# Optimization experiments

Measured on AMD Instinct MI355X. Metric: run time of the kernel, lower is better.

## Reference

```python
import jax, jax.numpy as jnp
import numpy as np
from jax import lax

V, E, Hd = 128, 256, 1024
B, S = 32, 1024

def setup_inputs() -> dict:
    key = jax.random.key(0)
    ks = jax.random.split(key, 10)
    s = 0.02
    return {
        "x": jax.random.randint(ks[0], (B, S), 0, V),
        "emb": jax.random.normal(ks[1], (V, E), jnp.float32) * s,
        "Wx_w": jax.random.normal(ks[2], (Hd, E), jnp.float32) * s,
        "Wx_b": jnp.zeros((Hd,), jnp.float32),
        "Wh_w": jax.random.normal(ks[3], (Hd, Hd), jnp.float32) * s,
        "Wh_b": jnp.zeros((Hd,), jnp.float32),
        "Wa_w": jax.random.normal(ks[4], (Hd, Hd), jnp.float32) * s,
        "Wa_b": jnp.zeros((Hd,), jnp.float32),
        "fc_w": jax.random.normal(ks[5], (V, 2 * Hd), jnp.float32) * s,
        "fc_b": jnp.zeros((V,), jnp.float32),
    }

def reference(x, emb, Wx_w, Wx_b, Wh_w, Wh_b, Wa_w, Wa_b, fc_w, fc_b):
    b, s = x.shape
    xe = emb[x]                                    # [B,S,E]
    Xp = jnp.einsum('bse,he->bsh', xe, Wx_w) + Wx_b  # precomputed input projection

    def step(h, xp_t):                             # h: [B,Hd], xp_t: [B,Hd]
        h2 = jnp.tanh(xp_t + h @ Wh_w.T + Wh_b)
        return h2, h2

    h0 = jnp.zeros((b, Wh_w.shape[0]), Xp.dtype)
    _, Hs = lax.scan(step, h0, Xp.transpose(1, 0, 2))  # [S,B,Hd]
    H = Hs.transpose(1, 0, 2)                      # [B,S,Hd]

    A = H @ Wa_w.T + Wa_b                          # W_a(H), computed once
    # scores[b,s,t] = A[b,s] . H[b,t]; key axis s, query axis t
    scores = jnp.einsum('bsh,bth->bst', A, H)
    allowed = jnp.triu(jnp.ones((s, s), bool))     # s <= t allowed (causal)
    scores = jnp.where(allowed[None], scores, -jnp.inf)
    weights = jax.nn.softmax(scores, axis=1)       # softmax over keys s
    context = jnp.einsum('bst,bsh->bth', weights, H)  # [B,S,Hd]

    combined = jnp.concatenate([H, context], axis=-1)  # [B,S,2Hd]
    return combined @ fc_w.T + fc_b                # [B,S,V]
```

## Files before the change

kernel.cpp:

```cpp
#include <hip/hip_runtime.h>
#include <hip/hip_bf16.h>
#include <hip/hip_cooperative_groups.h>

#define NV 128
#define NE 256
#define HD 1024
#define NB 32
#define NS 1024

typedef unsigned short u16;
typedef unsigned long long u64;
typedef unsigned short ushort8 __attribute__((ext_vector_type(8)));
typedef unsigned short u16x4 __attribute__((ext_vector_type(4)));
typedef short bf16x8 __attribute__((ext_vector_type(8)));
typedef float f32x4 __attribute__((ext_vector_type(4)));

#define MFMA16(a, b, c) __builtin_amdgcn_mfma_f32_16x16x32_bf16(a, b, c, 0, 0, 0)

__device__ __forceinline__ float bf2f(u16 u){
  unsigned int x = ((unsigned int)u) << 16;
  return __builtin_bit_cast(float, x);
}
__device__ __forceinline__ u16 f2bf(float f){
  unsigned int u = __builtin_bit_cast(unsigned int, f);
  unsigned int r = u + 0x7fffu + ((u >> 16) & 1u);
  return (u16)(r >> 16);
}

__global__ __launch_bounds__(256) void k_cvt(const float* __restrict__ waw,
    const float* __restrict__ fcw, u16* __restrict__ wa_bf, u16* __restrict__ fc_bf)
{
  const int i = blockIdx.x * 256 + threadIdx.x;
  if (i < 1048576) wa_bf[i] = f2bf(waw[i]);
  const int j = i - 1048576;
  if (j >= 0 && j < 262144) fc_bf[j] = f2bf(fcw[j]);
}

__global__ __launch_bounds__(256) void k_xw(const float* __restrict__ emb,
    const float* __restrict__ wxw, const float* __restrict__ wxb,
    float* __restrict__ XW)
{
  __shared__ float es[NE];
  const int v = blockIdx.x;
  for (int i = threadIdx.x; i < NE; i += 256) es[i] = emb[v*NE + i];
  __syncthreads();
  for (int h = threadIdx.x; h < HD; h += 256){
    const float* wr = wxw + (size_t)h * NE;
    float acc = 0.f;
#pragma unroll 4
    for (int e = 0; e < NE; e += 4){
      float4 w4 = *reinterpret_cast<const float4*>(wr + e);
      acc += w4.x*es[e] + w4.y*es[e+1] + w4.z*es[e+2] + w4.w*es[e+3];
    }
    XW[(size_t)v*HD + h] = acc + wxb[h];
  }
}

__global__ __launch_bounds__(256, 1) void k_scan2(const int* __restrict__ x,
    const float* __restrict__ whw, const float* __restrict__ whb,
    const float* __restrict__ XW, u64* __restrict__ hstate,
    u16* __restrict__ Harc)
{
  __shared__ __align__(16) float hs[4096];
  __shared__ int xs[4096];
  const int tid = threadIdx.x;
  const int g = blockIdx.x & 7;
  const int m = blockIdx.x >> 3;
  const int kc = tid & 31;
  const int rg = tid >> 5;
  const int row0 = m*32 + rg*4;

  for (int i = tid; i < 4096; i += 256) xs[i] = x[g*4096 + i];

  float4 wv[4][8];
#pragma unroll
  for (int r = 0; r < 4; ++r)
#pragma unroll
    for (int j = 0; j < 8; ++j)
      wv[r][j] = *reinterpret_cast<const float4*>(
          whw + (size_t)(row0 + r)*HD + kc*32 + ((4*(j + kc)) & 31));

  const int rr = row0 + (kc & 3);
  const int bb = kc >> 2;
  const float bias = whb[rr];
  __syncthreads();

  for (int t = 0; t < NS; ++t){
    const u64* hin  = hstate + (size_t)(t & 1)*(NB*HD) + g*4*HD;
    u64*       hout = hstate + (size_t)((t & 1)^1)*(NB*HD) + g*4*HD;
    const unsigned tg = (unsigned)t;
    u64 v[16];
#pragma unroll
    for (int q = 0; q < 16; ++q)
      v[q] = __hip_atomic_load(hin + q*256 + tid, __ATOMIC_RELAXED,
                               __HIP_MEMORY_SCOPE_AGENT);
    for (;;){
      bool ok = true;
#pragma unroll
      for (int q = 0; q < 16; ++q)
        if ((unsigned)(v[q] >> 32) != tg){
          ok = false;
          v[q] = __hip_atomic_load(hin + q*256 + tid, __ATOMIC_RELAXED,
                                   __HIP_MEMORY_SCOPE_AGENT);
        }
      if (ok) break;
      __builtin_amdgcn_s_sleep(1);
    }
#pragma unroll
    for (int q = 0; q < 16; ++q)
      hs[q*256 + tid] = __builtin_bit_cast(float, (unsigned)v[q]);
    float xwv = 0.f;
    if (kc < 16){
      const int xv = xs[bb*1024 + t];
      xwv = XW[(size_t)xv*HD + rr];
    }
    __syncthreads();

    float acc[4][4] = {};
#pragma unroll
    for (int j = 0; j < 8; ++j){
      const int off = kc*32 + ((4*(j + kc)) & 31);
      float4 h4[4];
#pragma unroll
      for (int b = 0; b < 4; ++b)
        h4[b] = *reinterpret_cast<const float4*>(&hs[b*1024 + off]);
#pragma unroll
      for (int r = 0; r < 4; ++r)
#pragma unroll
        for (int b = 0; b < 4; ++b)
          acc[r][b] += wv[r][j].x*h4[b].x + wv[r][j].y*h4[b].y
                     + wv[r][j].z*h4[b].z + wv[r][j].w*h4[b].w;
    }
#pragma unroll
    for (int mm = 1; mm <= 16; mm <<= 1)
#pragma unroll
      for (int r = 0; r < 4; ++r)
#pragma unroll
        for (int b = 0; b < 4; ++b)
          acc[r][b] += __shfl_xor(acc[r][b], mm);
    float sv = acc[0][0];
#pragma unroll
    for (int r = 0; r < 4; ++r)
#pragma unroll
      for (int b = 0; b < 4; ++b)
        if ((kc & 15) == b*4 + r) sv = acc[r][b];

    if (kc < 16){
      const float val = tanhf(xwv + bias + sv);
      const u64 pack = ((u64)(unsigned)(t + 1) << 32)
                     | (u64)__builtin_bit_cast(unsigned, val);
      __hip_atomic_store(&hout[bb*HD + rr], pack, __ATOMIC_RELAXED,
                         __HIP_MEMORY_SCOPE_AGENT);
      Harc[(((size_t)(g*4 + bb))*NS + t)*HD + rr] = f2bf(val);
    }
    __syncthreads();
  }
}

__global__ __launch_bounds__(256) void k_gemm_A(const u16* __restrict__ Harc,
    const u16* __restrict__ wa_bf, const float* __restrict__ wab,
    u16* __restrict__ Aarc)
{
  __shared__ u16 As[128][40];
  __shared__ u16 Bs[128][40];
  const int tid = threadIdx.x;
  const int m0 = blockIdx.x * 128;
  const int n0 = blockIdx.y * 128;
  const int l = tid & 63, w = tid >> 6;
  const int wr = w >> 1, wc = w & 1;
  const int lr = l & 15, lg = l >> 4;
  const int srow = tid >> 1, shalf = (tid & 1) * 16;
  f32x4 acc[4][4] = {};
  for (int k0 = 0; k0 < 1024; k0 += 32){
    {
      const u16* a = Harc + (size_t)(m0 + srow)*HD + k0 + shalf;
      ushort8 a0 = *(const ushort8*)a, a1 = *(const ushort8*)(a+8);
      const u16* b = wa_bf + (size_t)(n0 + srow)*HD + k0 + shalf;
      ushort8 b0 = *(const ushort8*)b, b1 = *(const ushort8*)(b+8);
      *(ushort8*)&As[srow][shalf] = a0; *(ushort8*)&As[srow][shalf+8] = a1;
      *(ushort8*)&Bs[srow][shalf] = b0; *(ushort8*)&Bs[srow][shalf+8] = b1;
    }
    __syncthreads();
    bf16x8 af[4], bfr[4];
#pragma unroll
    for (int i = 0; i < 4; ++i){
      af[i]  = *(const bf16x8*)&As[wr*64 + i*16 + lr][lg*8];
      bfr[i] = *(const bf16x8*)&Bs[wc*64 + i*16 + lr][lg*8];
    }
#pragma unroll
    for (int i = 0; i < 4; ++i)
#pragma unroll
      for (int j = 0; j < 4; ++j)
        acc[i][j] = MFMA16(af[i], bfr[j], acc[i][j]);
    __syncthreads();
  }
#pragma unroll
  for (int i = 0; i < 4; ++i){
    const int row = m0 + wr*64 + i*16 + lg*4;
#pragma unroll
    for (int j = 0; j < 4; ++j){
      const int col = n0 + wc*64 + j*16 + lr;
      const float bias = wab[col];
#pragma unroll
      for (int r = 0; r < 4; ++r)
        Aarc[(size_t)(row + r)*HD + col] = f2bf(acc[i][j][r] + bias);
    }
  }
}

__global__ __launch_bounds__(256) void k_scores(const u16* __restrict__ Harc,
    const u16* __restrict__ Aarc, u16* __restrict__ SW)
{
  if (blockIdx.x > blockIdx.y) return;
  __shared__ u16 As[128][40];
  __shared__ u16 Bs[128][40];
  const int tid = threadIdx.x;
  const int bz = blockIdx.z;
  const int m0 = blockIdx.y * 128;
  const int n0 = blockIdx.x * 128;
  const u16* Hb = Harc + (size_t)bz * NS * HD;
  const u16* Ab = Aarc + (size_t)bz * NS * HD;
  u16* Sb = SW + ((size_t)bz << 20);
  const int l = tid & 63, w = tid >> 6;
  const int wr = w >> 1, wc = w & 1;
  const int lr = l & 15, lg = l >> 4;
  const int srow = tid >> 1, shalf = (tid & 1) * 16;
  f32x4 acc[4][4] = {};
  for (int k0 = 0; k0 < 1024; k0 += 32){
    {
      const u16* a = Hb + (size_t)(m0 + srow)*HD + k0 + shalf;
      ushort8 a0 = *(const ushort8*)a, a1 = *(const ushort8*)(a+8);
      const u16* b = Ab + (size_t)(n0 + srow)*HD + k0 + shalf;
      ushort8 b0 = *(const ushort8*)b, b1 = *(const ushort8*)(b+8);
      *(ushort8*)&As[srow][shalf] = a0; *(ushort8*)&As[srow][shalf+8] = a1;
      *(ushort8*)&Bs[srow][shalf] = b0; *(ushort8*)&Bs[srow][shalf+8] = b1;
    }
    __syncthreads();
    bf16x8 af[4], bfr[4];
#pragma unroll
    for (int i = 0; i < 4; ++i){
      af[i]  = *(const bf16x8*)&As[wr*64 + i*16 + lr][lg*8];
      bfr[i] = *(const bf16x8*)&Bs[wc*64 + i*16 + lr][lg*8];
    }
#pragma unroll
    for (int i = 0; i < 4; ++i)
#pragma unroll
      for (int j = 0; j < 4; ++j)
        acc[i][j] = MFMA16(af[i], bfr[j], acc[i][j]);
    __syncthreads();
  }
#pragma unroll
  for (int i = 0; i < 4; ++i){
    const int row = m0 + wr*64 + i*16 + lg*4;
#pragma unroll
    for (int j = 0; j < 4; ++j){
      const int col = n0 + wc*64 + j*16 + lr;
#pragma unroll
      for (int r = 0; r < 4; ++r)
        Sb[((size_t)(row + r) << 10) + col] = f2bf(acc[i][j][r]);
    }
  }
}

__global__ __launch_bounds__(256) void k_softmax(u16* __restrict__ SW)
{
  const int bid = blockIdx.x;
  const int b = bid >> 10, t = bid & 1023;
  u16* row = SW + ((size_t)b << 20) + ((size_t)t << 10);
  const int i0 = threadIdx.x * 4;
  u16x4 v = *(const u16x4*)(row + i0);
  float x[4];
#pragma unroll
  for (int j = 0; j < 4; ++j) x[j] = (i0 + j <= t) ? bf2f(v[j]) : -1e30f;
  float m = fmaxf(fmaxf(x[0], x[1]), fmaxf(x[2], x[3]));
#pragma unroll
  for (int o = 1; o < 64; o <<= 1) m = fmaxf(m, __shfl_xor(m, o));
  __shared__ float redm[4], reds[4];
  if ((threadIdx.x & 63) == 0) redm[threadIdx.x >> 6] = m;
  __syncthreads();
  m = fmaxf(fmaxf(redm[0], redm[1]), fmaxf(redm[2], redm[3]));
  float e[4]; float s = 0.f;
#pragma unroll
  for (int j = 0; j < 4; ++j){ e[j] = __expf(x[j] - m); s += e[j]; }
#pragma unroll
  for (int o = 1; o < 64; o <<= 1) s += __shfl_xor(s, o);
  if ((threadIdx.x & 63) == 0) reds[threadIdx.x >> 6] = s;
  __syncthreads();
  s = reds[0] + reds[1] + reds[2] + reds[3];
  const float inv = 1.f / s;
  u16x4 o4;
#pragma unroll
  for (int j = 0; j < 4; ++j) o4[j] = f2bf(e[j] * inv);
  *(u16x4*)(row + i0) = o4;
}

__global__ __launch_bounds__(256) void k_pv(const u16* __restrict__ SW,
    const u16* __restrict__ Harc, u16* __restrict__ Ctx)
{
  __shared__ u16 As[128][40];
  __shared__ u16 Bs[128][40];
  const int tid = threadIdx.x;
  const int bz = blockIdx.z;
  const int t0 = blockIdx.x * 128;
  const int e0 = blockIdx.y * 128;
  const u16* Wb = SW + ((size_t)bz << 20);
  const u16* Hb = Harc + (size_t)bz * NS * HD;
  u16* Cb = Ctx + (size_t)bz * NS * HD;
  const int l = tid & 63, w = tid >> 6;
  const int wr = w >> 1, wc = w & 1;
  const int lr = l & 15, lg = l >> 4;
  const int srow = tid >> 1, shalf = (tid & 1) * 16;
  const int sIdx = tid & 31, ec = tid >> 5;
  const int ksteps = (blockIdx.x + 1) * 4;
  f32x4 acc[4][4] = {};
  for (int ks = 0; ks < ksteps; ++ks){
    const int k0 = ks * 32;
    {
      const u16* a = Wb + ((size_t)(t0 + srow) << 10) + k0 + shalf;
      ushort8 a0 = *(const ushort8*)a, a1 = *(const ushort8*)(a+8);
      const u16* b = Hb + (size_t)(k0 + sIdx)*HD + e0 + ec*16;
      ushort8 b0 = *(const ushort8*)b, b1 = *(const ushort8*)(b+8);
      *(ushort8*)&As[srow][shalf] = a0; *(ushort8*)&As[srow][shalf+8] = a1;
#pragma unroll
      for (int i = 0; i < 8; ++i){
        Bs[ec*16 + i][sIdx] = b0[i];
        Bs[ec*16 + 8 + i][sIdx] = b1[i];
      }
    }
    __syncthreads();
    bf16x8 af[4], bfr[4];
#pragma unroll
    for (int i = 0; i < 4; ++i){
      af[i]  = *(const bf16x8*)&As[wr*64 + i*16 + lr][lg*8];
      bfr[i] = *(const bf16x8*)&Bs[wc*64 + i*16 + lr][lg*8];
    }
#pragma unroll
    for (int i = 0; i < 4; ++i)
#pragma unroll
      for (int j = 0; j < 4; ++j)
        acc[i][j] = MFMA16(af[i], bfr[j], acc[i][j]);
    __syncthreads();
  }
#pragma unroll
  for (int i = 0; i < 4; ++i){
    const int row = t0 + wr*64 + i*16 + lg*4;
#pragma unroll
    for (int j = 0; j < 4; ++j){
      const int col = e0 + wc*64 + j*16 + lr;
#pragma unroll
      for (int r = 0; r < 4; ++r)
        Cb[(size_t)(row + r)*HD + col] = f2bf(acc[i][j][r]);
    }
  }
}

__global__ __launch_bounds__(256) void k_out2(const u16* __restrict__ Harc,
    const u16* __restrict__ Ctx, const u16* __restrict__ fc_bf,
    const float* __restrict__ fcb, float* __restrict__ out)
{
  __shared__ u16 As[128][40];
  __shared__ u16 Bs[128][40];
  const int tid = threadIdx.x;
  const int m0 = blockIdx.x * 128;
  const int l = tid & 63, w = tid >> 6;
  const int wr = w >> 1, wc = w & 1;
  const int lr = l & 15, lg = l >> 4;
  const int srow = tid >> 1, shalf = (tid & 1) * 16;
  f32x4 acc[4][4] = {};
  for (int k0 = 0; k0 < 2048; k0 += 32){
    {
      const u16* abase = (k0 < 1024) ? Harc : Ctx;
      const u16* a = abase + (size_t)(m0 + srow)*HD + (k0 & 1023) + shalf;
      ushort8 a0 = *(const ushort8*)a, a1 = *(const ushort8*)(a+8);
      const u16* b = fc_bf + (size_t)srow*2048 + k0 + shalf;
      ushort8 b0 = *(const ushort8*)b, b1 = *(const ushort8*)(b+8);
      *(ushort8*)&As[srow][shalf] = a0; *(ushort8*)&As[srow][shalf+8] = a1;
      *(ushort8*)&Bs[srow][shalf] = b0; *(ushort8*)&Bs[srow][shalf+8] = b1;
    }
    __syncthreads();
    bf16x8 af[4], bfr[4];
#pragma unroll
    for (int i = 0; i < 4; ++i){
      af[i]  = *(const bf16x8*)&As[wr*64 + i*16 + lr][lg*8];
      bfr[i] = *(const bf16x8*)&Bs[wc*64 + i*16 + lr][lg*8];
    }
#pragma unroll
    for (int i = 0; i < 4; ++i)
#pragma unroll
      for (int j = 0; j < 4; ++j)
        acc[i][j] = MFMA16(af[i], bfr[j], acc[i][j]);
    __syncthreads();
  }
#pragma unroll
  for (int i = 0; i < 4; ++i){
    const int row = m0 + wr*64 + i*16 + lg*4;
#pragma unroll
    for (int j = 0; j < 4; ++j){
      const int col = wc*64 + j*16 + lr;
      const float bias = fcb[col];
#pragma unroll
      for (int r = 0; r < 4; ++r)
        out[(size_t)(row + r)*NV + col] = acc[i][j][r] + bias;
    }
  }
}

extern "C" void kernel_launch(void* const* d_in, const int* in_sizes, int n_in,
                              void* d_out, int out_size, void* d_ws, size_t ws_size,
                              hipStream_t stream)
{
  const int*   x   = (const int*)  d_in[0];
  const float* emb = (const float*)d_in[1];
  const float* wxw = (const float*)d_in[2];
  const float* wxb = (const float*)d_in[3];
  const float* whw = (const float*)d_in[4];
  const float* whb = (const float*)d_in[5];
  const float* waw = (const float*)d_in[6];
  const float* wab = (const float*)d_in[7];
  const float* fcw = (const float*)d_in[8];
  const float* fcb = (const float*)d_in[9];
  float* out = (float*)d_out;

  char* ws = (char*)d_ws;
  u64*   hstate = (u64*)  (ws);
  float* XW     = (float*)(ws + 524288);
  u16*   Harc   = (u16*)  (ws + 1048576);
  u16*   Aarc   = (u16*)  (ws + 68157440);
  u16*   SW     = (u16*)  (ws + 135266304);
  u16*   wa_bf  = (u16*)  (ws + 135266304);
  u16*   fc_bf  = (u16*)  (ws + 202375168);
  u16*   Ctx    = Aarc;

  (void)hipMemsetAsync(ws, 0, 524288, stream);

  k_cvt<<<dim3(5120), dim3(256), 0, stream>>>(waw, fcw, wa_bf, fc_bf);
  k_xw<<<dim3(NV), dim3(256), 0, stream>>>(emb, wxw, wxb, XW);

  {
    void* args[] = { (void*)&x, (void*)&whw, (void*)&whb, (void*)&XW,
                     (void*)&hstate, (void*)&Harc };
    (void)hipLaunchCooperativeKernel((const void*)k_scan2, dim3(256), dim3(256),
                                     args, 0, stream);
  }

  k_gemm_A<<<dim3(256, 8), dim3(256), 0, stream>>>(Harc, wa_bf, wab, Aarc);
  k_scores<<<dim3(8, 8, 32), dim3(256), 0, stream>>>(Harc, Aarc, SW);
  k_softmax<<<dim3(32768), dim3(256), 0, stream>>>(SW);
  k_pv<<<dim3(8, 8, 32), dim3(256), 0, stream>>>(SW, Harc, Ctx);
  k_out2<<<dim3(256), dim3(256), 0, stream>>>(Harc, Ctx, fc_bf, fcb, out);
}
```

Measured before the change: 5.030 ms.

## Split scan batch group into two independent half-chains to overlap latency

Each block in the recurrent scan now handles its four batch rows as two independent pairs. For each pair it waits on that pair's hidden state, computes the matvec, and publishes the result before moving to the other pair. One half can then proceed while the other half's inputs are still arriving from other blocks, hiding some of the cross-block sync latency in the sequential scan. The change also raises the launch-bounds occupancy hint to 2. The risk is more polling rounds and barriers per step, and fewer independent FMAs per poll.

```diff
diff --git a/kernel.cpp b/kernel.cpp
--- a/kernel.cpp
+++ b/kernel.cpp
@@ -56,12 +56,13 @@
   }
 }
 
-__global__ __launch_bounds__(256, 1) void k_scan2(const int* __restrict__ x,
+__global__ __launch_bounds__(256, 2) void k_scan2(const int* __restrict__ x,
     const float* __restrict__ whw, const float* __restrict__ whb,
     const float* __restrict__ XW, u64* __restrict__ hstate,
     u16* __restrict__ Harc)
 {
-  __shared__ __align__(16) float hs[4096];
+  __shared__ __align__(16) float hsA[2048];
+  __shared__ __align__(16) float hsB[2048];
   __shared__ int xs[4096];
   const int tid = threadIdx.x;
   const int g = blockIdx.x & 7;
@@ -81,77 +82,139 @@
           whw + (size_t)(row0 + r)*HD + kc*32 + ((4*(j + kc)) & 31));
 
   const int rr = row0 + (kc & 3);
-  const int bb = kc >> 2;
+  const int bbp = (kc >> 2) & 1;
   const float bias = whb[rr];
   __syncthreads();
 
   for (int t = 0; t < NS; ++t){
-    const u64* hin  = hstate + (size_t)(t & 1)*(NB*HD) + g*4*HD;
-    u64*       hout = hstate + (size_t)((t & 1)^1)*(NB*HD) + g*4*HD;
     const unsigned tg = (unsigned)t;
-    u64 v[16];
-#pragma unroll
-    for (int q = 0; q < 16; ++q)
-      v[q] = __hip_atomic_load(hin + q*256 + tid, __ATOMIC_RELAXED,
-                               __HIP_MEMORY_SCOPE_AGENT);
-    for (;;){
-      bool ok = true;
-#pragma unroll
-      for (int q = 0; q < 16; ++q)
-        if ((unsigned)(v[q] >> 32) != tg){
-          ok = false;
-          v[q] = __hip_atomic_load(hin + q*256 + tid, __ATOMIC_RELAXED,
-                                   __HIP_MEMORY_SCOPE_AGENT);
+    const u64* hinA  = hstate + (size_t)(t & 1)*(NB*HD) + g*4096;
+    u64*       houtA = hstate + (size_t)((t & 1)^1)*(NB*HD) + g*4096;
+    const u64* hinB  = hinA + 2048;
+    u64*       houtB = houtA + 2048;
+
+    {
+      u64 v[8];
+#pragma unroll
+      for (int q = 0; q < 8; ++q)
+        v[q] = __hip_atomic_load(hinA + q*256 + tid, __ATOMIC_RELAXED,
+                                 __HIP_MEMORY_SCOPE_AGENT);
+      for (;;){
+        bool ok = true;
+#pragma unroll
+        for (int q = 0; q < 8; ++q)
+          if ((unsigned)(v[q] >> 32) != tg){
+            ok = false;
+            v[q] = __hip_atomic_load(hinA + q*256 + tid, __ATOMIC_RELAXED,
+                                     __HIP_MEMORY_SCOPE_AGENT);
+          }
+        if (ok) break;
+        __builtin_amdgcn_s_sleep(1);
+      }
+#pragma unroll
+      for (int q = 0; q < 8; ++q)
+        hsA[q*256 + tid] = __builtin_bit_cast(float, (unsigned)v[q]);
+      float xwv = 0.f;
+      if (kc < 8) xwv = XW[(size_t)xs[bbp*1024 + t]*HD + rr];
+      __syncthreads();
+
+      float acc[4][2] = {};
+#pragma unroll
+      for (int j = 0; j < 8; ++j){
+        const int off = kc*32 + ((4*(j + kc)) & 31);
+        float4 h0 = *reinterpret_cast<const float4*>(&hsA[off]);
+        float4 h1 = *reinterpret_cast<const float4*>(&hsA[1024 + off]);
+#pragma unroll
+        for (int r = 0; r < 4; ++r){
+          acc[r][0] += wv[r][j].x*h0.x + wv[r][j].y*h0.y
+                     + wv[r][j].z*h0.z + wv[r][j].w*h0.w;
+          acc[r][1] += wv[r][j].x*h1.x + wv[r][j].y*h1.y
+                     + wv[r][j].z*h1.z + wv[r][j].w*h1.w;
         }
-      if (ok) break;
-      __builtin_amdgcn_s_sleep(1);
-    }
-#pragma unroll
-    for (int q = 0; q < 16; ++q)
-      hs[q*256 + tid] = __builtin_bit_cast(float, (unsigned)v[q]);
-    float xwv = 0.f;
-    if (kc < 16){
-      const int xv = xs[bb*1024 + t];
-      xwv = XW[(size_t)xv*HD + rr];
-    }
-    __syncthreads();
-
-    float acc[4][4] = {};
-#pragma unroll
-    for (int j = 0; j < 8; ++j){
-      const int off = kc*32 + ((4*(j + kc)) & 31);
-      float4 h4[4];
-#pragma unroll
-      for (int b = 0; b < 4; ++b)
-        h4[b] = *reinterpret_cast<const float4*>(&hs[b*1024 + off]);
+      }
+#pragma unroll
+      for (int mm = 1; mm <= 16; mm <<= 1)
+#pragma unroll
+        for (int r = 0; r < 4; ++r){
+          acc[r][0] += __shfl_xor(acc[r][0], mm);
+          acc[r][1] += __shfl_xor(acc[r][1], mm);
+        }
+      float sv = acc[0][0];
 #pragma unroll
       for (int r = 0; r < 4; ++r)
 #pragma unroll
-        for (int b = 0; b < 4; ++b)
-          acc[r][b] += wv[r][j].x*h4[b].x + wv[r][j].y*h4[b].y
-                     + wv[r][j].z*h4[b].z + wv[r][j].w*h4[b].w;
-    }
-#pragma unroll
-    for (int mm = 1; mm <= 16; mm <<= 1)
+        for (int b = 0; b < 2; ++b)
+          if ((kc & 7) == b*4 + r) sv = acc[r][b];
+      if (kc < 8){
+        const float val = tanhf(xwv + bias + sv);
+        const u64 pack = ((u64)(unsigned)(t + 1) << 32)
+                       | (u64)__builtin_bit_cast(unsigned, val);
+        __hip_atomic_store(&houtA[bbp*1024 + rr], pack, __ATOMIC_RELAXED,
+                           __HIP_MEMORY_SCOPE_AGENT);
+        Harc[(((size_t)(g*4 + bbp))*NS + t)*HD + rr] = f2bf(val);
+      }
+    }
+
+    {
+      u64 v[8];
+#pragma unroll
+      for (int q = 0; q < 8; ++q)
+        v[q] = __hip_atomic_load(hinB + q*256 + tid, __ATOMIC_RELAXED,
+                                 __HIP_MEMORY_SCOPE_AGENT);
+      for (;;){
+        bool ok = true;
+#pragma unroll
+        for (int q = 0; q < 8; ++q)
+          if ((unsigned)(v[q] >> 32) != tg){
+            ok = false;
+            v[q] = __hip_atomic_load(hinB + q*256 + tid, __ATOMIC_RELAXED,
+                                     __HIP_MEMORY_SCOPE_AGENT);
+          }
+        if (ok) break;
+        __builtin_amdgcn_s_sleep(1);
+      }
+#pragma unroll
+      for (int q = 0; q < 8; ++q)
+        hsB[q*256 + tid] = __builtin_bit_cast(float, (unsigned)v[q]);
+      float xwv = 0.f;
+      if (kc < 8) xwv = XW[(size_t)xs[(2 + bbp)*1024 + t]*HD + rr];
+      __syncthreads();
+
+      float acc[4][2] = {};
+#pragma unroll
+      for (int j = 0; j < 8; ++j){
+        const int off = kc*32 + ((4*(j + kc)) & 31);
+        float4 h0 = *reinterpret_cast<const float4*>(&hsB[off]);
+        float4 h1 = *reinterpret_cast<const float4*>(&hsB[1024 + off]);
+#pragma unroll
+        for (int r = 0; r < 4; ++r){
+          acc[r][0] += wv[r][j].x*h0.x + wv[r][j].y*h0.y
+                     + wv[r][j].z*h0.z + wv[r][j].w*h0.w;
+          acc[r][1] += wv[r][j].x*h1.x + wv[r][j].y*h1.y
+                     + wv[r][j].z*h1.z + wv[r][j].w*h1.w;
+        }
+      }
+#pragma unroll
+      for (int mm = 1; mm <= 16; mm <<= 1)
+#pragma unroll
+        for (int r = 0; r < 4; ++r){
+          acc[r][0] += __shfl_xor(acc[r][0], mm);
+          acc[r][1] += __shfl_xor(acc[r][1], mm);
+        }
+      float sv = acc[0][0];
 #pragma unroll
       for (int r = 0; r < 4; ++r)
 #pragma unroll
-        for (int b = 0; b < 4; ++b)
-          acc[r][b] += __shfl_xor(acc[r][b], mm);
-    float sv = acc[0][0];
-#pragma unroll
-    for (int r = 0; r < 4; ++r)
-#pragma unroll
-      for (int b = 0; b < 4; ++b)
-        if ((kc & 15) == b*4 + r) sv = acc[r][b];
-
-    if (kc < 16){
-      const float val = tanhf(xwv + bias + sv);
-      const u64 pack = ((u64)(unsigned)(t + 1) << 32)
-                     | (u64)__builtin_bit_cast(unsigned, val);
-      __hip_atomic_store(&hout[bb*HD + rr], pack, __ATOMIC_RELAXED,
-                         __HIP_MEMORY_SCOPE_AGENT);
-      Harc[(((size_t)(g*4 + bb))*NS + t)*HD + rr] = f2bf(val);
+        for (int b = 0; b < 2; ++b)
+          if ((kc & 7) == b*4 + r) sv = acc[r][b];
+      if (kc < 8){
+        const float val = tanhf(xwv + bias + sv);
+        const u64 pack = ((u64)(unsigned)(t + 1) << 32)
+                       | (u64)__builtin_bit_cast(unsigned, val);
+        __hip_atomic_store(&houtB[bbp*1024 + rr], pack, __ATOMIC_RELAXED,
+                           __HIP_MEMORY_SCOPE_AGENT);
+        Harc[(((size_t)(g*4 + 2 + bbp))*NS + t)*HD + rr] = f2bf(val);
+      }
     }
     __syncthreads();
   }
```

Result: no change. 4.969 ms (-1.2%).
